# Kernel optimization log

Hardware: AMD Instinct MI355X
Metric: run time of the kernel (lower is better)

The kernel has to match this reference:

```python
import jax, jax.numpy as jnp
import numpy as np
from jax.ops import segment_sum

N_NODES = 100000
N_EDGES = 1600000
IN_DIM, HID_DIM, OUT_DIM = 256, 128, 237


def setup_inputs() -> dict:
    key = jax.random.key(0)
    ks = jax.random.split(key, 6)
    x = jax.random.normal(ks[0], (N_NODES, IN_DIM), dtype=jnp.float32)
    edge_index = jax.random.randint(ks[1], (2, N_EDGES), 0, N_NODES, dtype=jnp.int64)
    # Glorot-style init like PyG GCNConv
    W1 = jax.random.normal(ks[2], (IN_DIM, HID_DIM), dtype=jnp.float32) * (1.0 / np.sqrt(IN_DIM))
    b1 = jnp.zeros((HID_DIM,), dtype=jnp.float32)
    W2 = jax.random.normal(ks[3], (HID_DIM, OUT_DIM), dtype=jnp.float32) * (1.0 / np.sqrt(HID_DIM))
    b2 = jnp.zeros((OUT_DIM,), dtype=jnp.float32)
    return {"x": x, "edge_index": edge_index, "W1": W1, "b1": b1, "W2": W2, "b2": b2}


def _gcn_norm(edge_index, num_nodes):
    """Add self-loops and compute symmetric normalization deg^-1/2 * deg^-1/2."""
    loops = jnp.arange(num_nodes, dtype=edge_index.dtype)
    src = jnp.concatenate([edge_index[0], loops])
    dst = jnp.concatenate([edge_index[1], loops])
    deg = segment_sum(jnp.ones_like(dst, dtype=jnp.float32), dst, num_segments=num_nodes)
    dinv = jnp.where(deg > 0, jax.lax.rsqrt(deg), 0.0)
    norm = dinv[src] * dinv[dst]  # [E + N]
    return src, dst, norm


def _gcn_conv(h, src, dst, norm, W, b, num_nodes):
    # PyG GCNConv: linear transform first, then normalized scatter-add aggregation
    hw = h @ W                                   # [N, out]
    msg = hw[src] * norm[:, None]                # gather + scale, [E+N, out]
    out = segment_sum(msg, dst, num_segments=num_nodes)  # scatter-add into dst
    return out + b


def reference(x, edge_index, W1, b1, W2, b2):
    n = x.shape[0]
    src, dst, norm = _gcn_norm(edge_index, n)
    h = _gcn_conv(x, src, dst, norm, W1, b1, n)
    h = jax.nn.relu(h)
    out = _gcn_conv(h, src, dst, norm, W2, b2, n)
    return out
```

## Files before the change

kernel.cpp:

```cpp
#include <hip/hip_runtime.h>

#define N_NODES 100000
#define IN_DIM  256
#define HID_DIM 128
#define OUT_DIM 237

#define BSH   9
#define NBKT  196
#define BNODE 512

typedef __attribute__((ext_vector_type(8))) short bf16x8;
typedef __attribute__((ext_vector_type(4))) float fx4;
typedef __attribute__((ext_vector_type(8))) _Float16 h8;

__global__ __launch_bounds__(256) void k_bhist(const int* __restrict__ dst,
                                               int* __restrict__ bcnt, int E) {
    __shared__ int h[NBKT];
    for (int i = threadIdx.x; i < NBKT; i += 256) h[i] = 0;
    __syncthreads();
    const int base = blockIdx.x * 8192;
    for (int it = 0; it < 32; ++it) {
        int e = base + it * 256 + threadIdx.x;
        if (e < E) atomicAdd(&h[dst[e] >> BSH], 1);
    }
    __syncthreads();
    for (int i = threadIdx.x; i < NBKT; i += 256)
        if (h[i]) atomicAdd(&bcnt[i], h[i]);
}

__global__ void k_bscan(const int* __restrict__ bcnt, int* __restrict__ gbase,
                        int* __restrict__ gcur, int E) {
    __shared__ int lds[256];
    int tid = threadIdx.x;
    int v = (tid < NBKT) ? bcnt[tid] : 0;
    lds[tid] = v;
    __syncthreads();
    for (int off = 1; off < 256; off <<= 1) {
        int t = (tid >= off) ? lds[tid - off] : 0;
        __syncthreads();
        lds[tid] += t;
        __syncthreads();
    }
    int excl = lds[tid] - v;
    if (tid < NBKT) { gbase[tid] = excl; gcur[tid] = excl; }
    if (tid == 0) gbase[NBKT] = E;
}

__global__ __launch_bounds__(256) void k_part1(const int* __restrict__ src,
                                               const int* __restrict__ dst,
                                               int* __restrict__ gcur,
                                               int2* __restrict__ pairs, int E) {
    __shared__ int h[NBKT];
    __shared__ int base[NBKT];
    const int tid = threadIdx.x;
    for (int i = tid; i < NBKT; i += 256) h[i] = 0;
    __syncthreads();
    const int cbase = blockIdx.x * 8192;
    for (int it = 0; it < 32; ++it) {
        int e = cbase + it * 256 + tid;
        if (e < E) atomicAdd(&h[dst[e] >> BSH], 1);
    }
    __syncthreads();
    for (int i = tid; i < NBKT; i += 256) {
        int c = h[i];
        base[i] = c ? atomicAdd(&gcur[i], c) : 0;
    }
    __syncthreads();
    for (int i = tid; i < NBKT; i += 256) h[i] = 0;
    __syncthreads();
    for (int it = 0; it < 32; ++it) {
        int e = cbase + it * 256 + tid;
        if (e < E) {
            int d = dst[e];
            int b = d >> BSH;
            int pos = base[b] + atomicAdd(&h[b], 1);
            pairs[pos] = make_int2(src[e], d);
        }
    }
}

__global__ __launch_bounds__(256) void k_bucket_csr(const int2* __restrict__ pairs,
                                                    const int* __restrict__ gbase,
                                                    int* __restrict__ rp,
                                                    float* __restrict__ dinv,
                                                    int* __restrict__ ss, int n, int E) {
    __shared__ int cnt[BNODE];
    __shared__ int excl[BNODE];
    __shared__ int sbuf[256];
    const int b = blockIdx.x;
    const int n0 = b << BSH;
    const int tid = threadIdx.x;
    for (int i = tid; i < BNODE; i += 256) cnt[i] = 0;
    __syncthreads();
    const int beg = gbase[b], end = gbase[b + 1];
    for (int i = beg + tid; i < end; i += 256)
        atomicAdd(&cnt[pairs[i].y - n0], 1);
    __syncthreads();
    int c0 = cnt[2 * tid], c1 = cnt[2 * tid + 1];
    int s = c0 + c1;
    sbuf[tid] = s;
    __syncthreads();
    for (int off = 1; off < 256; off <<= 1) {
        int t = (tid >= off) ? sbuf[tid - off] : 0;
        __syncthreads();
        sbuf[tid] += t;
        __syncthreads();
    }
    int e0 = sbuf[tid] - s;
    excl[2 * tid] = e0;
    excl[2 * tid + 1] = e0 + c0;
    __syncthreads();
    for (int i = tid; i < BNODE; i += 256) {
        int node = n0 + i;
        if (node < n) {
            rp[node] = beg + excl[i];
            dinv[node] = rsqrtf((float)cnt[i] + 1.0f);
        }
    }
    __syncthreads();
    for (int i = tid; i < BNODE; i += 256) cnt[i] = beg + excl[i];
    __syncthreads();
    for (int i = beg + tid; i < end; i += 256) {
        int2 p = pairs[i];
        int pos = atomicAdd(&cnt[p.y - n0], 1);
        ss[pos] = p.x;
    }
    if (b == 0 && tid == 0) rp[n] = E;
}

__global__ __launch_bounds__(256) void k_wsplit(const float* __restrict__ W,
                                                unsigned short* __restrict__ Wh,
                                                unsigned short* __restrict__ Wl,
                                                int K, int C, int CD) {
    int t = blockIdx.x * 256 + threadIdx.x;
    if (t >= K * CD) return;
    int k = t / CD, c = t - k * CD;
    float v = (c < C) ? W[k * C + c] : 0.f;
    unsigned u = __float_as_uint(v);
    unsigned short hi = (unsigned short)(u >> 16);
    float lof = v - __uint_as_float(u & 0xffff0000u);
    unsigned short lo = (unsigned short)(__float_as_uint(lof) >> 16);
    int d = ((k >> 3) * CD + c) * 8 + (k & 7);
    Wh[d] = hi;
    Wl[d] = lo;
}

template <typename AT, typename OT, int K, int CD, int SCALE, int BIAS>
__global__ __launch_bounds__(256) void k_gemm_mfma(const AT* __restrict__ A,
                                                   const unsigned short* __restrict__ Bh,
                                                   const unsigned short* __restrict__ Bl,
                                                   const float* __restrict__ dinv,
                                                   const float* __restrict__ bias,
                                                   OT* __restrict__ out,
                                                   int ldo, int ncol) {
    const int tid = threadIdx.x;
    const int lane = tid & 63;
    const int w = tid >> 6;
    const int l15 = lane & 15;
    const int lq = lane >> 4;
    const int rowbase = blockIdx.x * 128 + w * 32;
    const int col0 = blockIdx.y * 128;

    const bf16x8* __restrict__ Bh8 = (const bf16x8*)Bh;
    const bf16x8* __restrict__ Bl8 = (const bf16x8*)Bl;

    fx4 acc[2][8] = {};

    for (int k0 = 0; k0 < K; k0 += 32) {
        bf16x8 ah[2], al[2];
#pragma unroll
        for (int rf = 0; rf < 2; ++rf) {
            int row = rowbase + rf * 16 + l15;
            if (row > N_NODES - 1) row = N_NODES - 1;
            const AT* ap = A + (size_t)row * K + k0 + lq * 8;
            float f[8];
            if constexpr (sizeof(AT) == 4) {
                float4 f0 = *(const float4*)ap;
                float4 f1 = *(const float4*)(ap + 4);
                f[0] = f0.x; f[1] = f0.y; f[2] = f0.z; f[3] = f0.w;
                f[4] = f1.x; f[5] = f1.y; f[6] = f1.z; f[7] = f1.w;
            } else {
                h8 v = *(const h8*)ap;
#pragma unroll
                for (int i = 0; i < 8; ++i) f[i] = (float)v[i];
            }
#pragma unroll
            for (int i = 0; i < 8; ++i) {
                unsigned u = __float_as_uint(f[i]);
                ah[rf][i] = (short)(u >> 16);
                float lof = f[i] - __uint_as_float(u & 0xffff0000u);
                al[rf][i] = (short)(__float_as_uint(lof) >> 16);
            }
        }
        const int kb = (k0 >> 3) + lq;
#pragma unroll
        for (int cf = 0; cf < 8; ++cf) {
            const int bi = kb * CD + col0 + cf * 16 + l15;
            bf16x8 bh = Bh8[bi];
            bf16x8 bl = Bl8[bi];
#pragma unroll
            for (int rf = 0; rf < 2; ++rf) {
                acc[rf][cf] = __builtin_amdgcn_mfma_f32_16x16x32_bf16(ah[rf], bh, acc[rf][cf], 0, 0, 0);
                acc[rf][cf] = __builtin_amdgcn_mfma_f32_16x16x32_bf16(ah[rf], bl, acc[rf][cf], 0, 0, 0);
                acc[rf][cf] = __builtin_amdgcn_mfma_f32_16x16x32_bf16(al[rf], bh, acc[rf][cf], 0, 0, 0);
            }
        }
    }

    float bb[8];
#pragma unroll
    for (int cf = 0; cf < 8; ++cf) {
        int c = col0 + cf * 16 + l15;
        bb[cf] = (BIAS && c < ncol) ? bias[c] : 0.f;
    }

#pragma unroll
    for (int rf = 0; rf < 2; ++rf) {
#pragma unroll
        for (int r = 0; r < 4; ++r) {
            const int row = rowbase + rf * 16 + lq * 4 + r;
            if (row < N_NODES) {
                const float s = SCALE ? dinv[row] : 1.f;
#pragma unroll
                for (int cf = 0; cf < 8; ++cf) {
                    const int c = col0 + cf * 16 + l15;
                    if (c < ncol) {
                        float v = acc[rf][cf][r];
                        if (SCALE) v *= s;
                        if (BIAS) v += bb[cf];
                        out[(size_t)row * ldo + c] = (OT)v;
                    }
                }
            }
        }
    }
}

template <int RELU, typename OT>
__global__ __launch_bounds__(256) void k_agg_csr(const _Float16* __restrict__ tab,
                                                 const int* __restrict__ rp,
                                                 const int* __restrict__ ss,
                                                 const float* __restrict__ dinv,
                                                 const float* __restrict__ bias,
                                                 OT* __restrict__ outp, int n) {
    int t = blockIdx.x * 256 + threadIdx.x;
    int node = t >> 4;
    int q = (t & 15) * 8;
    if (node >= n) return;
    int beg = rp[node], end = rp[node + 1];
    float a[8] = {};
    int i = beg;
    for (; i + 2 <= end; i += 2) {
        int s0 = ss[i], s1 = ss[i + 1];
        h8 v0 = *(const h8*)(tab + (size_t)s0 * HID_DIM + q);
        h8 v1 = *(const h8*)(tab + (size_t)s1 * HID_DIM + q);
#pragma unroll
        for (int j = 0; j < 8; ++j) a[j] += (float)v0[j] + (float)v1[j];
    }
    if (i < end) {
        int s0 = ss[i];
        h8 v0 = *(const h8*)(tab + (size_t)s0 * HID_DIM + q);
#pragma unroll
        for (int j = 0; j < 8; ++j) a[j] += (float)v0[j];
    }
    h8 own = *(const h8*)(tab + (size_t)node * HID_DIM + q);
    float s = dinv[node];
    if constexpr (RELU) {
        float4 b0 = *(const float4*)(bias + q);
        float4 b1 = *(const float4*)(bias + q + 4);
        float bb[8] = {b0.x, b0.y, b0.z, b0.w, b1.x, b1.y, b1.z, b1.w};
        h8 r;
#pragma unroll
        for (int j = 0; j < 8; ++j)
            r[j] = (_Float16)(fmaxf(fmaf(s, a[j] + (float)own[j], bb[j]), 0.f) * s);
        *(h8*)((_Float16*)outp + (size_t)node * HID_DIM + q) = r;
    } else if constexpr (sizeof(OT) == 2) {
        h8 r;
#pragma unroll
        for (int j = 0; j < 8; ++j) r[j] = (_Float16)(s * (a[j] + (float)own[j]));
        *(h8*)((_Float16*)outp + (size_t)node * HID_DIM + q) = r;
    } else {
        float* op = (float*)outp + (size_t)node * HID_DIM + q;
        float4 r0, r1;
        r0.x = s * (a[0] + (float)own[0]);
        r0.y = s * (a[1] + (float)own[1]);
        r0.z = s * (a[2] + (float)own[2]);
        r0.w = s * (a[3] + (float)own[3]);
        r1.x = s * (a[4] + (float)own[4]);
        r1.y = s * (a[5] + (float)own[5]);
        r1.z = s * (a[6] + (float)own[6]);
        r1.w = s * (a[7] + (float)own[7]);
        *(float4*)op = r0;
        *(float4*)(op + 4) = r1;
    }
}

__global__ __launch_bounds__(256) void k_gemm2(const float* __restrict__ A2,
                                               const float* __restrict__ W2,
                                               const float* __restrict__ b2,
                                               float* __restrict__ out) {
    __shared__ float As[16 * 132];
    __shared__ float Bs[16 * 128];
    const int tid = threadIdx.x;
    const int tx = tid & 15, ty = tid >> 4;
    const int row0 = blockIdx.x * 128;
    const int col0 = blockIdx.y * 128;

    const int ar = tid >> 2;
    const int ak = (tid & 3) * 4;
    const int bk = tid >> 5;
    const int bc = (tid & 31) * 4;

    float acc[8][8] = {};

    for (int k0 = 0; k0 < HID_DIM; k0 += 16) {
        float4 a0 = make_float4(0.f, 0.f, 0.f, 0.f), a1 = a0;
        const int r0 = row0 + ar, r1 = row0 + ar + 64;
        if (r0 < N_NODES) a0 = *(const float4*)(A2 + (size_t)r0 * HID_DIM + k0 + ak);
        if (r1 < N_NODES) a1 = *(const float4*)(A2 + (size_t)r1 * HID_DIM + k0 + ak);
        float bv0[4], bv1[4];
#pragma unroll
        for (int j = 0; j < 4; ++j) {
            int c = col0 + bc + j;
            bv0[j] = (c < OUT_DIM) ? W2[(size_t)(k0 + bk) * OUT_DIM + c] : 0.f;
            bv1[j] = (c < OUT_DIM) ? W2[(size_t)(k0 + bk + 8) * OUT_DIM + c] : 0.f;
        }
        __syncthreads();
        As[(ak + 0) * 132 + ar] = a0.x;
        As[(ak + 1) * 132 + ar] = a0.y;
        As[(ak + 2) * 132 + ar] = a0.z;
        As[(ak + 3) * 132 + ar] = a0.w;
        As[(ak + 0) * 132 + ar + 64] = a1.x;
        As[(ak + 1) * 132 + ar + 64] = a1.y;
        As[(ak + 2) * 132 + ar + 64] = a1.z;
        As[(ak + 3) * 132 + ar + 64] = a1.w;
#pragma unroll
        for (int j = 0; j < 4; ++j) {
            Bs[bk * 128 + bc + j] = bv0[j];
            Bs[(bk + 8) * 128 + bc + j] = bv1[j];
        }
        __syncthreads();
#pragma unroll
        for (int kk = 0; kk < 16; ++kk) {
            float4 A0 = *(const float4*)(As + kk * 132 + ty * 4);
            float4 A1 = *(const float4*)(As + kk * 132 + 64 + ty * 4);
            float4 B0 = *(const float4*)(Bs + kk * 128 + tx * 4);
            float4 B1 = *(const float4*)(Bs + kk * 128 + 64 + tx * 4);
            float a_[8] = {A0.x, A0.y, A0.z, A0.w, A1.x, A1.y, A1.z, A1.w};
            float b_[8] = {B0.x, B0.y, B0.z, B0.w, B1.x, B1.y, B1.z, B1.w};
#pragma unroll
            for (int i = 0; i < 8; ++i)
#pragma unroll
                for (int j = 0; j < 8; ++j)
                    acc[i][j] = fmaf(a_[i], b_[j], acc[i][j]);
        }
    }
#pragma unroll
    for (int i = 0; i < 8; ++i) {
        const int r = row0 + ty * 4 + (i & 3) + (i >> 2) * 64;
        if (r < N_NODES) {
#pragma unroll
            for (int j = 0; j < 8; ++j) {
                int c = col0 + tx * 4 + (j & 3) + (j >> 2) * 64;
                if (c < OUT_DIM) out[(size_t)r * OUT_DIM + c] = acc[i][j] + b2[c];
            }
        }
    }
}

extern "C" void kernel_launch(void* const* d_in, const int* in_sizes, int n_in,
                              void* d_out, int out_size, void* d_ws, size_t ws_size,
                              hipStream_t stream) {
    const float* x  = (const float*)d_in[0];
    const int*   ei = (const int*)d_in[1];
    const float* W1 = (const float*)d_in[2];
    const float* b1 = (const float*)d_in[3];
    const float* W2 = (const float*)d_in[4];
    const float* b2 = (const float*)d_in[5];
    float* out = (float*)d_out;

    const int E = in_sizes[1] / 2;
    const int* src = ei;
    const int* dst = ei + E;

    _Float16* hs = (_Float16*)d_ws;
    _Float16* A2h = hs;
    float* A2f = (float*)d_ws;

    char* ob = (char*)d_out;
    size_t o = (size_t)N_NODES * HID_DIM * 2;
    _Float16* h2 = (_Float16*)ob;
    float* dinv = (float*)(ob + o); o += 400128;
    int* bcnt = (int*)(ob + o); o += 1024;
    int* rp   = (int*)(ob + o); o += 400640;
    int* gbase = (int*)(ob + o); o += 1024;
    int* gcur  = (int*)(ob + o); o += 1024;
    int* ss   = (int*)(ob + o); o += (size_t)E * 4;
    int2* pairs = (int2*)(ob + o); o += (size_t)E * 8;
    unsigned short* W1h = (unsigned short*)(ob + o); o += 65536;
    unsigned short* W1l = (unsigned short*)(ob + o); o += 65536;

    const size_t W2OFF = 32u << 20;
    const bool w2frag = ws_size >= W2OFF + 131072;
    unsigned short* W2h = (unsigned short*)((char*)d_ws + W2OFF);
    unsigned short* W2l = W2h + 32768;

    const int NB1 = (E + 8191) / 8192;

    k_wsplit<<<128, 256, 0, stream>>>(W1, W1h, W1l, IN_DIM, HID_DIM, HID_DIM);
    if (w2frag)
        k_wsplit<<<128, 256, 0, stream>>>(W2, W2h, W2l, HID_DIM, OUT_DIM, 256);

    hipMemsetAsync(bcnt, 0, 1024, stream);
    k_bhist<<<NB1, 256, 0, stream>>>(dst, bcnt, E);
    k_bscan<<<1, 256, 0, stream>>>(bcnt, gbase, gcur, E);
    k_part1<<<NB1, 256, 0, stream>>>(src, dst, gcur, pairs, E);
    k_bucket_csr<<<NBKT, 256, 0, stream>>>(pairs, gbase, rp, dinv, ss, N_NODES, E);

    dim3 g1((N_NODES + 127) / 128, 1);
    k_gemm_mfma<float, _Float16, IN_DIM, HID_DIM, 1, 0><<<g1, 256, 0, stream>>>(
        x, W1h, W1l, dinv, nullptr, hs, HID_DIM, HID_DIM);

    const int aggBlocks = (N_NODES * 16 + 255) / 256;
    k_agg_csr<1, _Float16><<<aggBlocks, 256, 0, stream>>>(hs, rp, ss, dinv, b1, h2, N_NODES);

    if (w2frag) {
        k_agg_csr<0, _Float16><<<aggBlocks, 256, 0, stream>>>(h2, rp, ss, dinv, b1, A2h, N_NODES);
        dim3 g2((N_NODES + 127) / 128, 2);
        k_gemm_mfma<_Float16, float, HID_DIM, 256, 0, 1><<<g2, 256, 0, stream>>>(
            A2h, W2h, W2l, nullptr, b2, out, OUT_DIM, OUT_DIM);
    } else {
        k_agg_csr<0, float><<<aggBlocks, 256, 0, stream>>>(h2, rp, ss, dinv, b1, A2f, N_NODES);
        dim3 g2((N_NODES + 127) / 128, (OUT_DIM + 127) / 128);
        k_gemm2<<<g2, 256, 0, stream>>>(A2f, W2, b2, out);
    }
}
```

Before: 488.3 us.

## Stage B weight tiles in LDS and prefetch A rows one k-step ahead

The MFMA GEMM kernel now copies the block's full hi/lo bf16 weight slice into shared memory once, then reads B fragments from LDS instead of global memory in the inner loop. It also software-pipelines the A-operand loads, fetching the next k-step's fp32/fp16 row data before the split-and-MFMA work on the current one. The aim is to cut repeated global B traffic and hide A load latency. In exchange it uses a large LDS buffer (K=256 gives 128 KB), which limits occupancy, and adds registers for the prefetch buffer.

```diff
diff --git a/kernel.cpp b/kernel.cpp
--- a/kernel.cpp
+++ b/kernel.cpp
@@ -153,6 +153,10 @@
                                                    const float* __restrict__ bias,
                                                    OT* __restrict__ out,
                                                    int ldo, int ncol) {
+    constexpr int NS = K / 32;
+    constexpr int NSLOT = (K / 8) * 2 * 128;
+    __shared__ bf16x8 Blds[NSLOT];
+
     const int tid = threadIdx.x;
     const int lane = tid & 63;
     const int w = tid >> 6;
@@ -164,40 +168,63 @@
     const bf16x8* __restrict__ Bh8 = (const bf16x8*)Bh;
     const bf16x8* __restrict__ Bl8 = (const bf16x8*)Bl;
 
+    for (int idx = tid; idx < NSLOT; idx += 256) {
+        int c = idx & 127;
+        int hl = (idx >> 7) & 1;
+        int kb = idx >> 8;
+        Blds[idx] = (hl ? Bl8 : Bh8)[kb * CD + col0 + c];
+    }
+    __syncthreads();
+
+    int r0 = rowbase + l15;      if (r0 > N_NODES - 1) r0 = N_NODES - 1;
+    int r1 = rowbase + 16 + l15; if (r1 > N_NODES - 1) r1 = N_NODES - 1;
+    const AT* ap0 = A + (size_t)r0 * K + lq * 8;
+    const AT* ap1 = A + (size_t)r1 * K + lq * 8;
+
     fx4 acc[2][8] = {};
-
-    for (int k0 = 0; k0 < K; k0 += 32) {
+    float af[2][8];
+
+#define LDA(dst_, ptr_, ks_)                                              \
+    do {                                                                  \
+        const AT* p_ = (ptr_) + (ks_) * 32;                               \
+        if constexpr (sizeof(AT) == 4) {                                  \
+            float4 f0_ = *(const float4*)p_;                              \
+            float4 f1_ = *(const float4*)(p_ + 4);                        \
+            dst_[0] = f0_.x; dst_[1] = f0_.y; dst_[2] = f0_.z;            \
+            dst_[3] = f0_.w; dst_[4] = f1_.x; dst_[5] = f1_.y;            \
+            dst_[6] = f1_.z; dst_[7] = f1_.w;                             \
+        } else {                                                          \
+            h8 v_ = *(const h8*)p_;                                       \
+            _Pragma("unroll")                                             \
+            for (int i_ = 0; i_ < 8; ++i_) dst_[i_] = (float)v_[i_];      \
+        }                                                                 \
+    } while (0)
+
+    LDA(af[0], ap0, 0);
+    LDA(af[1], ap1, 0);
+
+    for (int ks = 0; ks < NS; ++ks) {
+        float fn[2][8];
+        if (ks + 1 < NS) {
+            LDA(fn[0], ap0, ks + 1);
+            LDA(fn[1], ap1, ks + 1);
+        }
         bf16x8 ah[2], al[2];
 #pragma unroll
-        for (int rf = 0; rf < 2; ++rf) {
-            int row = rowbase + rf * 16 + l15;
-            if (row > N_NODES - 1) row = N_NODES - 1;
-            const AT* ap = A + (size_t)row * K + k0 + lq * 8;
-            float f[8];
-            if constexpr (sizeof(AT) == 4) {
-                float4 f0 = *(const float4*)ap;
-                float4 f1 = *(const float4*)(ap + 4);
-                f[0] = f0.x; f[1] = f0.y; f[2] = f0.z; f[3] = f0.w;
-                f[4] = f1.x; f[5] = f1.y; f[6] = f1.z; f[7] = f1.w;
-            } else {
-                h8 v = *(const h8*)ap;
-#pragma unroll
-                for (int i = 0; i < 8; ++i) f[i] = (float)v[i];
-            }
+        for (int rf = 0; rf < 2; ++rf)
 #pragma unroll
             for (int i = 0; i < 8; ++i) {
-                unsigned u = __float_as_uint(f[i]);
+                float fv = af[rf][i];
+                unsigned u = __float_as_uint(fv);
                 ah[rf][i] = (short)(u >> 16);
-                float lof = f[i] - __uint_as_float(u & 0xffff0000u);
+                float lof = fv - __uint_as_float(u & 0xffff0000u);
                 al[rf][i] = (short)(__float_as_uint(lof) >> 16);
             }
-        }
-        const int kb = (k0 >> 3) + lq;
+        const int kb = ks * 4 + lq;
 #pragma unroll
         for (int cf = 0; cf < 8; ++cf) {
-            const int bi = kb * CD + col0 + cf * 16 + l15;
-            bf16x8 bh = Bh8[bi];
-            bf16x8 bl = Bl8[bi];
+            bf16x8 bh = Blds[(kb * 2 + 0) * 128 + cf * 16 + l15];
+            bf16x8 bl = Blds[(kb * 2 + 1) * 128 + cf * 16 + l15];
 #pragma unroll
             for (int rf = 0; rf < 2; ++rf) {
                 acc[rf][cf] = __builtin_amdgcn_mfma_f32_16x16x32_bf16(ah[rf], bh, acc[rf][cf], 0, 0, 0);
@@ -205,7 +232,14 @@
                 acc[rf][cf] = __builtin_amdgcn_mfma_f32_16x16x32_bf16(al[rf], bh, acc[rf][cf], 0, 0, 0);
             }
         }
-    }
+        if (ks + 1 < NS) {
+#pragma unroll
+            for (int rf = 0; rf < 2; ++rf)
+#pragma unroll
+                for (int i = 0; i < 8; ++i) af[rf][i] = fn[rf][i];
+        }
+    }
+#undef LDA
 
     float bb[8];
 #pragma unroll
```

New measurement: 546.3 us. +11.9%, slower.

## Reuse per-block histograms, pack edge pairs into 32 bits, halve partition block size

Applied to the files above, without the earlier changes.

The bucket-histogram kernel now stores each block's per-bucket counts, so the partition kernel reads them instead of recounting, which removes its second pass over dst. Edge pairs are packed into one 32-bit word (src shifted left by 9, low 9 bits the node offset within the bucket) instead of an int2, halving the traffic for writing and reading pairs. Edges per block drop from 8192 to 4096, doubling the grid for better parallelism at the cost of more global atomics on the bucket cursors and a larger per-block histogram array. Packing assumes src fits in 23 bits, which holds for 100000 nodes.

```diff
diff --git a/kernel.cpp b/kernel.cpp
--- a/kernel.cpp
+++ b/kernel.cpp
@@ -8,24 +8,30 @@
 #define BSH   9
 #define NBKT  196
 #define BNODE 512
+#define EPB   4096
 
 typedef __attribute__((ext_vector_type(8))) short bf16x8;
 typedef __attribute__((ext_vector_type(4))) float fx4;
 typedef __attribute__((ext_vector_type(8))) _Float16 h8;
 
 __global__ __launch_bounds__(256) void k_bhist(const int* __restrict__ dst,
-                                               int* __restrict__ bcnt, int E) {
+                                               int* __restrict__ bcnt,
+                                               int* __restrict__ hcnt, int E) {
     __shared__ int h[NBKT];
     for (int i = threadIdx.x; i < NBKT; i += 256) h[i] = 0;
     __syncthreads();
-    const int base = blockIdx.x * 8192;
-    for (int it = 0; it < 32; ++it) {
+    const int base = blockIdx.x * EPB;
+    for (int it = 0; it < EPB / 256; ++it) {
         int e = base + it * 256 + threadIdx.x;
         if (e < E) atomicAdd(&h[dst[e] >> BSH], 1);
     }
     __syncthreads();
-    for (int i = threadIdx.x; i < NBKT; i += 256)
-        if (h[i]) atomicAdd(&bcnt[i], h[i]);
+    int* hrow = hcnt + blockIdx.x * NBKT;
+    for (int i = threadIdx.x; i < NBKT; i += 256) {
+        int c = h[i];
+        hrow[i] = c;
+        if (c) atomicAdd(&bcnt[i], c);
+    }
 }
 
 __global__ void k_bscan(const int* __restrict__ bcnt, int* __restrict__ gbase,
@@ -48,38 +54,32 @@
 
 __global__ __launch_bounds__(256) void k_part1(const int* __restrict__ src,
                                                const int* __restrict__ dst,
+                                               const int* __restrict__ hcnt,
                                                int* __restrict__ gcur,
-                                               int2* __restrict__ pairs, int E) {
+                                               unsigned* __restrict__ pairs, int E) {
     __shared__ int h[NBKT];
     __shared__ int base[NBKT];
     const int tid = threadIdx.x;
-    for (int i = tid; i < NBKT; i += 256) h[i] = 0;
-    __syncthreads();
-    const int cbase = blockIdx.x * 8192;
-    for (int it = 0; it < 32; ++it) {
-        int e = cbase + it * 256 + tid;
-        if (e < E) atomicAdd(&h[dst[e] >> BSH], 1);
-    }
-    __syncthreads();
+    const int* hrow = hcnt + blockIdx.x * NBKT;
     for (int i = tid; i < NBKT; i += 256) {
-        int c = h[i];
+        int c = hrow[i];
         base[i] = c ? atomicAdd(&gcur[i], c) : 0;
-    }
-    __syncthreads();
-    for (int i = tid; i < NBKT; i += 256) h[i] = 0;
-    __syncthreads();
-    for (int it = 0; it < 32; ++it) {
+        h[i] = 0;
+    }
+    __syncthreads();
+    const int cbase = blockIdx.x * EPB;
+    for (int it = 0; it < EPB / 256; ++it) {
         int e = cbase + it * 256 + tid;
         if (e < E) {
             int d = dst[e];
             int b = d >> BSH;
             int pos = base[b] + atomicAdd(&h[b], 1);
-            pairs[pos] = make_int2(src[e], d);
-        }
-    }
-}
-
-__global__ __launch_bounds__(256) void k_bucket_csr(const int2* __restrict__ pairs,
+            pairs[pos] = ((unsigned)src[e] << BSH) | (unsigned)(d & (BNODE - 1));
+        }
+    }
+}
+
+__global__ __launch_bounds__(256) void k_bucket_csr(const unsigned* __restrict__ pairs,
                                                     const int* __restrict__ gbase,
                                                     int* __restrict__ rp,
                                                     float* __restrict__ dinv,
@@ -94,7 +94,7 @@
     __syncthreads();
     const int beg = gbase[b], end = gbase[b + 1];
     for (int i = beg + tid; i < end; i += 256)
-        atomicAdd(&cnt[pairs[i].y - n0], 1);
+        atomicAdd(&cnt[pairs[i] & (BNODE - 1)], 1);
     __syncthreads();
     int c0 = cnt[2 * tid], c1 = cnt[2 * tid + 1];
     int s = c0 + c1;
@@ -121,9 +121,9 @@
     for (int i = tid; i < BNODE; i += 256) cnt[i] = beg + excl[i];
     __syncthreads();
     for (int i = beg + tid; i < end; i += 256) {
-        int2 p = pairs[i];
-        int pos = atomicAdd(&cnt[p.y - n0], 1);
-        ss[pos] = p.x;
+        unsigned p = pairs[i];
+        int pos = atomicAdd(&cnt[p & (BNODE - 1)], 1);
+        ss[pos] = (int)(p >> BSH);
     }
     if (b == 0 && tid == 0) rp[n] = E;
 }
@@ -387,6 +387,8 @@
     _Float16* A2h = hs;
     float* A2f = (float*)d_ws;
 
+    const int NB1 = (E + EPB - 1) / EPB;
+
     char* ob = (char*)d_out;
     size_t o = (size_t)N_NODES * HID_DIM * 2;
     _Float16* h2 = (_Float16*)ob;
@@ -396,7 +398,8 @@
     int* gbase = (int*)(ob + o); o += 1024;
     int* gcur  = (int*)(ob + o); o += 1024;
     int* ss   = (int*)(ob + o); o += (size_t)E * 4;
-    int2* pairs = (int2*)(ob + o); o += (size_t)E * 8;
+    unsigned* pairs = (unsigned*)(ob + o); o += (size_t)E * 4;
+    int* hcnt = (int*)(ob + o); o += (size_t)NB1 * NBKT * 4;
     unsigned short* W1h = (unsigned short*)(ob + o); o += 65536;
     unsigned short* W1l = (unsigned short*)(ob + o); o += 65536;
 
@@ -405,16 +408,14 @@
     unsigned short* W2h = (unsigned short*)((char*)d_ws + W2OFF);
     unsigned short* W2l = W2h + 32768;
 
-    const int NB1 = (E + 8191) / 8192;
-
     k_wsplit<<<128, 256, 0, stream>>>(W1, W1h, W1l, IN_DIM, HID_DIM, HID_DIM);
     if (w2frag)
         k_wsplit<<<128, 256, 0, stream>>>(W2, W2h, W2l, HID_DIM, OUT_DIM, 256);
 
     hipMemsetAsync(bcnt, 0, 1024, stream);
-    k_bhist<<<NB1, 256, 0, stream>>>(dst, bcnt, E);
+    k_bhist<<<NB1, 256, 0, stream>>>(dst, bcnt, hcnt, E);
     k_bscan<<<1, 256, 0, stream>>>(bcnt, gbase, gcur, E);
-    k_part1<<<NB1, 256, 0, stream>>>(src, dst, gcur, pairs, E);
+    k_part1<<<NB1, 256, 0, stream>>>(src, dst, hcnt, gcur, pairs, E);
     k_bucket_csr<<<NBKT, 256, 0, stream>>>(pairs, gbase, rp, dinv, ss, N_NODES, E);
 
     dim3 g1((N_NODES + 127) / 128, 1);
```

After: 478.0 us. -2.1%, faster.
